# Kernel tuning notes

Measured on AMD Instinct MI355X. Metric: run time of the kernel, lower is better.

Reference implementation:

```python
import jax, jax.numpy as jnp
import numpy as np

FEAT = 512
COND = 768
N_HEADS = 8
D_HEAD = 64
D_ATTN = N_HEADS * D_HEAD  # 512


def setup_inputs() -> dict:
    key = jax.random.key(0)
    ks = jax.random.split(key, 8)
    B, N, M = 16, 4096, 77
    x = jax.random.normal(ks[0], (B, N, FEAT), dtype=jnp.float32)
    cond = jax.random.normal(ks[1], (B, M, COND), dtype=jnp.float32)
    s_f = 1.0 / np.sqrt(FEAT)
    s_c = 1.0 / np.sqrt(COND)
    s_a = 1.0 / np.sqrt(D_ATTN)
    Wq = jax.random.normal(ks[2], (FEAT, D_ATTN), dtype=jnp.float32) * s_f
    Wk = jax.random.normal(ks[3], (COND, D_ATTN), dtype=jnp.float32) * s_c
    Wv = jax.random.normal(ks[4], (COND, D_ATTN), dtype=jnp.float32) * s_c
    Wo = jax.random.normal(ks[5], (D_ATTN, FEAT), dtype=jnp.float32) * s_a
    bo = jax.random.normal(ks[6], (FEAT,), dtype=jnp.float32) * 0.01
    return {"x": x, "cond": cond, "Wq": Wq, "Wk": Wk, "Wv": Wv, "Wo": Wo, "bo": bo}


def reference(x, cond, Wq, Wk, Wv, Wo, bo):
    B, N, _ = x.shape
    M = cond.shape[1]
    scale = D_HEAD ** (-0.5)
    # projections (no bias, as in nn.Linear(..., bias=False))
    q = (x @ Wq).reshape(B, N, N_HEADS, D_HEAD)
    k = (cond @ Wk).reshape(B, M, N_HEADS, D_HEAD)
    v = (cond @ Wv).reshape(B, M, N_HEADS, D_HEAD)
    attn = jnp.einsum('bihd,bjhd->bhij', q, k) * scale  # [B,H,N,M]
    attn = jax.nn.softmax(attn, axis=-1)  # split-half inplace softmax == plain softmax
    out = jnp.einsum('bhij,bjhd->bihd', attn, v).reshape(B, N, D_ATTN)
    return out @ Wo + bo
```

## Files before the change

kernel.cpp:

```cpp
#include <hip/hip_runtime.h>

typedef __attribute__((ext_vector_type(8))) _Float16 f16x8;
typedef __attribute__((ext_vector_type(4))) float f32x4;

#define B_SZ   16
#define N_SEQ  4096
#define M_CTX  77
#define M_PAD  96
#define NH     8

__device__ __forceinline__ _Float16 f2h(float x) { return (_Float16)x; }

__device__ __forceinline__ void gload16(const void* g, void* l) {
    __builtin_amdgcn_global_load_lds(
        (const __attribute__((address_space(1))) unsigned int*)g,
        (__attribute__((address_space(3))) unsigned int*)l, 16, 0, 0);
}

#define BAR()   asm volatile("s_barrier" ::: "memory")
#define WAITV2() asm volatile("s_waitcnt vmcnt(2)" ::: "memory")
#define WAITV0() asm volatile("s_waitcnt vmcnt(0)" ::: "memory")

template<int C>
__device__ __forceinline__ float dppf(float x) {
    union { float f; int i; } u, v;
    u.f = x;
    v.i = __builtin_amdgcn_mov_dpp(u.i, C, 0xF, 0xF, true);
    return v.f;
}
__device__ __forceinline__ float rmax16(float x) {
    x = fmaxf(x, dppf<0xB1>(x));
    x = fmaxf(x, dppf<0x4E>(x));
    x = fmaxf(x, dppf<0x141>(x));
    x = fmaxf(x, dppf<0x140>(x));
    return x;
}
__device__ __forceinline__ float rsum16(float x) {
    x += dppf<0xB1>(x);
    x += dppf<0x4E>(x);
    x += dppf<0x141>(x);
    x += dppf<0x140>(x);
    return x;
}

__global__ __launch_bounds__(256)
void convert(const float4* __restrict__ x, f16x8* __restrict__ xh, int n8)
{
    int idx = blockIdx.x * 256 + threadIdx.x;
    int stride = gridDim.x * 256;
    for (int i = idx; i < n8; i += stride) {
        float4 a = x[2 * i];
        float4 b = x[2 * i + 1];
        f16x8 o;
        o[0] = f2h(a.x); o[1] = f2h(a.y); o[2] = f2h(a.z); o[3] = f2h(a.w);
        o[4] = f2h(b.x); o[5] = f2h(b.y); o[6] = f2h(b.z); o[7] = f2h(b.w);
        xh[i] = o;
    }
}

__global__ __launch_bounds__(256)
void prep(const float* __restrict__ Wq, const float* __restrict__ Wk,
          const float* __restrict__ Wv, const float* __restrict__ Wo,
          _Float16* __restrict__ WqT, _Float16* __restrict__ WkT,
          _Float16* __restrict__ WvT, _Float16* __restrict__ WoT)
{
    __shared__ float t[32][33];
    const float* W; _Float16* WT; int K; float scale = 1.0f;
    switch (blockIdx.z) {
        case 0:  W = Wq; WT = WqT; K = 512; scale = 0.125f; break;
        case 1:  W = Wk; WT = WkT; K = 768; break;
        case 2:  W = Wv; WT = WvT; K = 768; break;
        default: W = Wo; WT = WoT; K = 512; break;
    }
    const int ky = blockIdx.y;
    if (ky * 32 >= K) return;
    const int nx = blockIdx.x;
    const int tr = threadIdx.x >> 5, tc = threadIdx.x & 31;
#pragma unroll
    for (int i = 0; i < 4; ++i) {
        int kr = tr + i * 8;
        t[kr][tc] = W[(size_t)(ky * 32 + kr) * 512 + nx * 32 + tc];
    }
    __syncthreads();
#pragma unroll
    for (int i = 0; i < 4; ++i) {
        int nr = tr + i * 8;
        WT[(size_t)(nx * 32 + nr) * K + ky * 32 + tc] = f2h(t[tc][nr] * scale);
    }
}

__global__ __launch_bounds__(256)
void kv_proj(const float* __restrict__ cond, const _Float16* __restrict__ WkT,
             const _Float16* __restrict__ WvT, _Float16* __restrict__ Kswz,
             _Float16* __restrict__ Vswz)
{
    const int tid = threadIdx.x;
    const int l = tid & 63, w = tid >> 6;
    const int lrow = l & 15, lk = l >> 4;
    const int h = blockIdx.x, b = blockIdx.y, which = blockIdx.z;
    const _Float16* WT = which ? WvT : WkT;
    const float* cb = cond + (size_t)b * M_CTX * 768;

    f32x4 acc[5];
#pragma unroll
    for (int i = 0; i < 5; ++i)
#pragma unroll
        for (int e = 0; e < 4; ++e) acc[i][e] = 0.f;

    const int n = h * 64 + w * 16 + lrow;
    for (int kk = 0; kk < 24; ++kk) {
        f16x8 bfrag = *(const f16x8*)(WT + (size_t)n * 768 + kk * 32 + lk * 8);
#pragma unroll
        for (int rt = 0; rt < 5; ++rt) {
            int m = rt * 16 + lrow;
            f16x8 afrag;
#pragma unroll
            for (int j = 0; j < 8; ++j) afrag[j] = (_Float16)0.f;
            if (m < M_CTX) {
                const float* a = cb + (size_t)m * 768 + kk * 32 + lk * 8;
                float4 f0 = *(const float4*)a;
                float4 f1 = *(const float4*)(a + 4);
                afrag[0] = f2h(f0.x); afrag[1] = f2h(f0.y);
                afrag[2] = f2h(f0.z); afrag[3] = f2h(f0.w);
                afrag[4] = f2h(f1.x); afrag[5] = f2h(f1.y);
                afrag[6] = f2h(f1.z); afrag[7] = f2h(f1.w);
            }
            acc[rt] = __builtin_amdgcn_mfma_f32_16x16x32_f16(afrag, bfrag, acc[rt], 0, 0, 0);
        }
    }

    const int bh = b * NH + h;
    const int d = w * 16 + lrow;
    const int dhi = d >> 3, dlo = d & 7;
    if (which == 0) {
        _Float16* Kb = Kswz + (size_t)bh * (M_PAD * 64);
#pragma unroll
        for (int rt = 0; rt < 5; ++rt)
#pragma unroll
            for (int r = 0; r < 4; ++r) {
                int m = rt * 16 + lk * 4 + r;
                Kb[m * 64 + ((dhi ^ (m & 7)) * 8) + dlo] = f2h(acc[rt][r]);
            }
#pragma unroll
        for (int r = 0; r < 4; ++r) {
            int m = 80 + lk * 4 + r;
            Kb[m * 64 + ((dhi ^ (m & 7)) * 8) + dlo] = (_Float16)0.f;
        }
    } else {
        _Float16* Vb = Vswz + (size_t)bh * (64 * 128);
#pragma unroll
        for (int rt = 0; rt < 5; ++rt)
#pragma unroll
            for (int r = 0; r < 4; ++r) {
                int m = rt * 16 + lk * 4 + r;
                Vb[d * 128 + (((m >> 3) ^ dlo) * 8) + (m & 7)] = f2h(acc[rt][r]);
            }
#pragma unroll
        for (int r = 0; r < 4; ++r) {
            int m = 80 + lk * 4 + r;
            Vb[d * 128 + (((m >> 3) ^ dlo) * 8) + (m & 7)] = (_Float16)0.f;
        }
    }
}

template<int EMODE>
__global__ __launch_bounds__(512, 2)
void gemm256(const _Float16* __restrict__ A, const _Float16* __restrict__ BT,
             void* __restrict__ Cv, const float* __restrict__ bias)
{
    __shared__ _Float16 As[32768];
    __shared__ _Float16 Bs[32768];

    const int bid = blockIdx.x;
    const int wg = (bid & 7) * 64 + (bid >> 3);
    const int rb = wg >> 1, cb = wg & 1;
    const size_t row0 = (size_t)rb * 256;
    const int col0 = cb * 256;

    const int tid = threadIdx.x;
    const int l = tid & 63, w = tid >> 6;
    const int wy = w >> 2, wx = w & 3;
    const int lrow = l & 15, lk = l >> 4;

    f32x4 acc[8][4];
#pragma unroll
    for (int i = 0; i < 8; ++i)
#pragma unroll
        for (int j = 0; j < 4; ++j)
#pragma unroll
            for (int e = 0; e < 4; ++e) acc[i][j][e] = 0.f;

    const _Float16* a_src = A + (row0 + (size_t)(tid >> 2)) * 512 + (tid & 3) * 8;
    const _Float16* b_src = BT + (size_t)(col0 + (tid >> 2)) * 512 + (tid & 3) * 8;
    _Float16* As_d = &As[w * 512];
    _Float16* Bs_d = &Bs[w * 512];

    auto stageA = [&](int t) {
        const _Float16* s = a_src + t * 32;
        _Float16* d = As_d + (t & 1) * 8192;
        gload16(s, d);
        gload16(s + 128 * 512, d + 4096);
    };
    auto stageB = [&](int t) {
        const _Float16* s = b_src + t * 32;
        _Float16* d = Bs_d + (t & 1) * 8192;
        gload16(s, d);
        gload16(s + 128 * 512, d + 4096);
    };

    stageA(0); stageB(0); stageB(1);
    WAITV2();
    BAR();

    const _Float16* Ar = &As[wy * 4096 + lrow * 32 + lk * 8];
    const _Float16* Br = &Bs[(wx >> 1) * 4096 + ((wx & 1) * 64 + lrow) * 32 + lk * 8];

    for (int t = 0; t < 16; ++t) {
        const int bo = (t & 1) * 8192;
        f16x8 af[4], bf[4];
#pragma unroll
        for (int i = 0; i < 4; ++i) af[i] = *(const f16x8*)(Ar + bo + i * 512);
#pragma unroll
        for (int i = 0; i < 4; ++i) bf[i] = *(const f16x8*)(Br + bo + i * 512);
        if (t + 1 < 16) stageA(t + 1);
        BAR();
        __builtin_amdgcn_s_setprio(1);
#pragma unroll
        for (int mt = 0; mt < 4; ++mt)
#pragma unroll
            for (int nt = 0; nt < 4; ++nt)
                acc[mt][nt] = __builtin_amdgcn_mfma_f32_16x16x32_f16(af[mt], bf[nt], acc[mt][nt], 0, 0, 0);
        __builtin_amdgcn_s_setprio(0);

        f16x8 ag[4];
#pragma unroll
        for (int i = 0; i < 4; ++i) ag[i] = *(const f16x8*)(Ar + bo + (4 + i) * 512);
        if (t + 2 < 16) stageB(t + 2);
        __builtin_amdgcn_s_setprio(1);
#pragma unroll
        for (int mt = 0; mt < 4; ++mt)
#pragma unroll
            for (int nt = 0; nt < 4; ++nt)
                acc[4 + mt][nt] = __builtin_amdgcn_mfma_f32_16x16x32_f16(ag[mt], bf[nt], acc[4 + mt][nt], 0, 0, 0);
        __builtin_amdgcn_s_setprio(0);

        if (t <= 13)      WAITV2();
        else if (t == 14) WAITV0();
        if (t < 15) BAR();
    }

#pragma unroll
    for (int mt = 0; mt < 8; ++mt)
#pragma unroll
        for (int nt = 0; nt < 4; ++nt)
#pragma unroll
            for (int r = 0; r < 4; ++r) {
                size_t row = row0 + wy * 128 + mt * 16 + lk * 4 + r;
                int col = col0 + wx * 64 + nt * 16 + lrow;
                float v = acc[mt][nt][r];
                if (EMODE == 0) {
                    ((_Float16*)Cv)[row * 512 + col] = f2h(v);
                } else {
                    ((float*)Cv)[row * 512 + col] = v + bias[col];
                }
            }
}

__global__ __launch_bounds__(256)
void attn(const _Float16* __restrict__ Q, const _Float16* __restrict__ Kswz,
          const _Float16* __restrict__ Vswz, _Float16* __restrict__ AO)
{
    __shared__ _Float16 Ks[M_PAD * 64];
    __shared__ _Float16 Vs[64 * 128];
    __shared__ _Float16 Pl[4][16][104];

    const int tid = threadIdx.x;
    const int l = tid & 63, w = tid >> 6;
    const int lrow = l & 15, lk = l >> 4;
    const int chunk = blockIdx.x, h = blockIdx.y, b = blockIdx.z;
    const int bh = b * NH + h;

    {
        const _Float16* Kg = Kswz + (size_t)bh * (M_PAD * 64);
        const _Float16* Vg = Vswz + (size_t)bh * (64 * 128);
#pragma unroll
        for (int i = 0; i < 3; ++i) {
            int c = w * 3 + i;
            gload16(Kg + c * 512 + l * 8, Ks + c * 512);
        }
#pragma unroll
        for (int i = 0; i < 4; ++i) {
            int c = w * 4 + i;
            gload16(Vg + c * 512 + l * 8, Vs + c * 512);
        }
    }

    const size_t row0 = (size_t)b * N_SEQ + chunk * 256 + w * 64;
    f16x8 af[4][2];
    {
        const _Float16* Qb = Q + (row0 + lrow) * 512 + h * 64 + lk * 8;
#pragma unroll
        for (int mt = 0; mt < 4; ++mt)
#pragma unroll
            for (int kk = 0; kk < 2; ++kk)
                af[mt][kk] = *(const f16x8*)(Qb + (size_t)mt * 16 * 512 + kk * 32);
    }

    for (int idx = l; idx < 256; idx += 64)
        Pl[w][idx >> 4][80 + (idx & 15)] = (_Float16)0.f;

    __syncthreads();

    const bool m4ok = (lrow < 13);
    const int kswz = lrow & 7;

#pragma unroll
    for (int mt = 0; mt < 4; ++mt) {
        f32x4 s[5];
#pragma unroll
        for (int i = 0; i < 5; ++i)
#pragma unroll
            for (int e = 0; e < 4; ++e) s[i][e] = 0.f;
#pragma unroll
        for (int kk = 0; kk < 2; ++kk)
#pragma unroll
            for (int ct = 0; ct < 5; ++ct) {
                f16x8 kf = *(const f16x8*)&Ks[(ct * 16 + lrow) * 64 + (((kk * 4 + lk) ^ kswz) * 8)];
                s[ct] = __builtin_amdgcn_mfma_f32_16x16x32_f16(af[mt][kk], kf, s[ct], 0, 0, 0);
            }

        float rinv[4];
#pragma unroll
        for (int r = 0; r < 4; ++r) {
            float v0 = s[0][r], v1 = s[1][r], v2 = s[2][r], v3 = s[3][r], v4 = s[4][r];
            float mx = fmaxf(fmaxf(v0, v1), fmaxf(v2, v3));
            mx = fmaxf(mx, m4ok ? v4 : -1e30f);
            mx = rmax16(mx);
            float e0 = __expf(v0 - mx), e1 = __expf(v1 - mx);
            float e2 = __expf(v2 - mx), e3 = __expf(v3 - mx);
            float e4 = m4ok ? __expf(v4 - mx) : 0.f;
            float sum = ((e0 + e1) + (e2 + e3)) + e4;
            sum = rsum16(sum);
            rinv[r] = 1.0f / sum;
            int prow = lk * 4 + r;
            Pl[w][prow][lrow]      = f2h(e0);
            Pl[w][prow][16 + lrow] = f2h(e1);
            Pl[w][prow][32 + lrow] = f2h(e2);
            Pl[w][prow][48 + lrow] = f2h(e3);
            Pl[w][prow][64 + lrow] = f2h(e4);
        }

        f32x4 o[4];
#pragma unroll
        for (int i = 0; i < 4; ++i)
#pragma unroll
            for (int e2 = 0; e2 < 4; ++e2) o[i][e2] = 0.f;
#pragma unroll
        for (int kk = 0; kk < 3; ++kk) {
            f16x8 pa = *(const f16x8*)&Pl[w][lrow][kk * 32 + lk * 8];
#pragma unroll
            for (int ctd = 0; ctd < 4; ++ctd) {
                f16x8 vf = *(const f16x8*)&Vs[(ctd * 16 + lrow) * 128 + (((kk * 4 + lk) ^ kswz) * 8)];
                o[ctd] = __builtin_amdgcn_mfma_f32_16x16x32_f16(pa, vf, o[ctd], 0, 0, 0);
            }
        }

        const size_t rw = row0 + mt * 16 + lk * 4;
#pragma unroll
        for (int ctd = 0; ctd < 4; ++ctd)
#pragma unroll
            for (int r = 0; r < 4; ++r)
                AO[(rw + r) * 512 + h * 64 + ctd * 16 + lrow] = f2h(o[ctd][r] * rinv[r]);
    }
}

extern "C" void kernel_launch(void* const* d_in, const int* in_sizes, int n_in,
                              void* d_out, int out_size, void* d_ws, size_t ws_size,
                              hipStream_t stream)
{
    (void)in_sizes; (void)n_in; (void)out_size; (void)ws_size;
    const float* x    = (const float*)d_in[0];
    const float* cond = (const float*)d_in[1];
    const float* Wq   = (const float*)d_in[2];
    const float* Wk   = (const float*)d_in[3];
    const float* Wv   = (const float*)d_in[4];
    const float* Wo   = (const float*)d_in[5];
    const float* bo   = (const float*)d_in[6];

    char* ws = (char*)d_ws;
    _Float16* WqT  = (_Float16*)(ws);
    _Float16* WoT  = (_Float16*)(ws + 524288);
    _Float16* Kswz = (_Float16*)(ws + 1048576);
    _Float16* Vswz = (_Float16*)(ws + 2621440);
    _Float16* xh   = (_Float16*)(ws + 4718592);
    _Float16* WkT  = (_Float16*)(ws + 4718592);
    _Float16* WvT  = (_Float16*)(ws + 4718592 + 786432);
    _Float16* AO   = xh;
    _Float16* Qf   = (_Float16*)d_out;

    prep<<<dim3(16, 24, 4), 256, 0, stream>>>(Wq, Wk, Wv, Wo, WqT, WkT, WvT, WoT);
    kv_proj<<<dim3(8, 16, 2), 256, 0, stream>>>(cond, WkT, WvT, Kswz, Vswz);
    convert<<<dim3(2048), 256, 0, stream>>>((const float4*)x, (f16x8*)xh, 16 * 4096 * 512 / 8);
    gemm256<0><<<dim3(512), 512, 0, stream>>>(xh, WqT, Qf, nullptr);
    attn<<<dim3(16, 8, 16), 256, 0, stream>>>(Qf, Kswz, Vswz, AO);
    gemm256<1><<<dim3(512), 512, 0, stream>>>(AO, WoT, d_out, bo);
}
```

Before: 229.4 us.

## Replace double-buffered GEMM with 4-stage LDS ring and swizzled layout

Rewrites the projection GEMM main loop to use a four-deep LDS ring that prefetches three k-tiles ahead, with one wait and barrier per k-step instead of split A/B staging with two barriers. LDS rows use a rotated slot swizzle to reduce bank conflicts on fragment reads. All eight A fragments are loaded at once, which raises register pressure. The fixed vmcnt(8) wait may not fully drain loads in the last iterations, so the tail carries a synchronization risk.

```diff
diff --git a/kernel.cpp b/kernel.cpp
--- a/kernel.cpp
+++ b/kernel.cpp
@@ -17,9 +17,8 @@
         (__attribute__((address_space(3))) unsigned int*)l, 16, 0, 0);
 }
 
-#define BAR()   asm volatile("s_barrier" ::: "memory")
-#define WAITV2() asm volatile("s_waitcnt vmcnt(2)" ::: "memory")
-#define WAITV0() asm volatile("s_waitcnt vmcnt(0)" ::: "memory")
+#define BAR()    asm volatile("s_barrier" ::: "memory")
+#define WAITV8() asm volatile("s_waitcnt vmcnt(8)" ::: "memory")
 
 template<int C>
 __device__ __forceinline__ float dppf(float x) {
@@ -164,24 +163,38 @@
 }
 
 template<int EMODE>
-__global__ __launch_bounds__(512, 2)
-void gemm256(const _Float16* __restrict__ A, const _Float16* __restrict__ BT,
-             void* __restrict__ Cv, const float* __restrict__ bias)
-{
-    __shared__ _Float16 As[32768];
-    __shared__ _Float16 Bs[32768];
+__global__ __launch_bounds__(512)
+void gemm_pipe(const _Float16* __restrict__ A, const _Float16* __restrict__ BT,
+               void* __restrict__ Cv, const float* __restrict__ bias)
+{
+    __shared__ _Float16 L[4 * 16384];
 
     const int bid = blockIdx.x;
     const int wg = (bid & 7) * 64 + (bid >> 3);
-    const int rb = wg >> 1, cb = wg & 1;
-    const size_t row0 = (size_t)rb * 256;
-    const int col0 = cb * 256;
+    const size_t row0 = (size_t)(wg >> 1) * 256;
+    const int col0 = (wg & 1) * 256;
 
     const int tid = threadIdx.x;
     const int l = tid & 63, w = tid >> 6;
     const int wy = w >> 2, wx = w & 3;
     const int lrow = l & 15, lk = l >> 4;
 
+    const int srow  = l >> 2;
+    const int sslot = ((l & 3) - srow) & 3;
+    const _Float16* a_src = A  + (row0 + (size_t)(w * 32 + srow)) * 512 + sslot * 8;
+    const _Float16* b_src = BT + ((size_t)col0 + w * 32 + srow) * 512 + sslot * 8;
+
+    auto stage = [&](int t) {
+        _Float16* dA = &L[(t & 3) * 16384 + w * 1024];
+        _Float16* dB = dA + 8192;
+        const _Float16* sA = a_src + t * 32;
+        const _Float16* sB = b_src + t * 32;
+        gload16(sA,            dA);
+        gload16(sA + 16 * 512, dA + 512);
+        gload16(sB,            dB);
+        gload16(sB + 16 * 512, dB + 512);
+    };
+
     f32x4 acc[8][4];
 #pragma unroll
     for (int i = 0; i < 8; ++i)
@@ -190,63 +203,33 @@
 #pragma unroll
             for (int e = 0; e < 4; ++e) acc[i][j][e] = 0.f;
 
-    const _Float16* a_src = A + (row0 + (size_t)(tid >> 2)) * 512 + (tid & 3) * 8;
-    const _Float16* b_src = BT + (size_t)(col0 + (tid >> 2)) * 512 + (tid & 3) * 8;
-    _Float16* As_d = &As[w * 512];
-    _Float16* Bs_d = &Bs[w * 512];
-
-    auto stageA = [&](int t) {
-        const _Float16* s = a_src + t * 32;
-        _Float16* d = As_d + (t & 1) * 8192;
-        gload16(s, d);
-        gload16(s + 128 * 512, d + 4096);
-    };
-    auto stageB = [&](int t) {
-        const _Float16* s = b_src + t * 32;
-        _Float16* d = Bs_d + (t & 1) * 8192;
-        gload16(s, d);
-        gload16(s + 128 * 512, d + 4096);
-    };
-
-    stageA(0); stageB(0); stageB(1);
-    WAITV2();
-    BAR();
-
-    const _Float16* Ar = &As[wy * 4096 + lrow * 32 + lk * 8];
-    const _Float16* Br = &Bs[(wx >> 1) * 4096 + ((wx & 1) * 64 + lrow) * 32 + lk * 8];
-
-    for (int t = 0; t < 16; ++t) {
-        const int bo = (t & 1) * 8192;
-        f16x8 af[4], bf[4];
-#pragma unroll
-        for (int i = 0; i < 4; ++i) af[i] = *(const f16x8*)(Ar + bo + i * 512);
-#pragma unroll
-        for (int i = 0; i < 4; ++i) bf[i] = *(const f16x8*)(Br + bo + i * 512);
-        if (t + 1 < 16) stageA(t + 1);
+    stage(0); stage(1); stage(2);
+
+    const int rdoff = ((lk + lrow) & 3) * 8;
+    const int aoff = (wy * 128 + lrow) * 32 + rdoff;
+    const int boff = 8192 + (wx * 64 + lrow) * 32 + rdoff;
+
+    for (int kt = 0; kt < 16; ++kt) {
+        WAITV8();
         BAR();
+        if (kt + 3 < 16) stage(kt + 3);
+
+        const _Float16* Lb = &L[(kt & 3) * 16384];
+        f16x8 af[8], bf[4];
+#pragma unroll
+        for (int mt = 0; mt < 8; ++mt)
+            af[mt] = *(const f16x8*)(Lb + aoff + mt * 512);
+#pragma unroll
+        for (int nt = 0; nt < 4; ++nt)
+            bf[nt] = *(const f16x8*)(Lb + boff + nt * 512);
+
         __builtin_amdgcn_s_setprio(1);
 #pragma unroll
-        for (int mt = 0; mt < 4; ++mt)
+        for (int mt = 0; mt < 8; ++mt)
 #pragma unroll
             for (int nt = 0; nt < 4; ++nt)
                 acc[mt][nt] = __builtin_amdgcn_mfma_f32_16x16x32_f16(af[mt], bf[nt], acc[mt][nt], 0, 0, 0);
         __builtin_amdgcn_s_setprio(0);
-
-        f16x8 ag[4];
-#pragma unroll
-        for (int i = 0; i < 4; ++i) ag[i] = *(const f16x8*)(Ar + bo + (4 + i) * 512);
-        if (t + 2 < 16) stageB(t + 2);
-        __builtin_amdgcn_s_setprio(1);
-#pragma unroll
-        for (int mt = 0; mt < 4; ++mt)
-#pragma unroll
-            for (int nt = 0; nt < 4; ++nt)
-                acc[4 + mt][nt] = __builtin_amdgcn_mfma_f32_16x16x32_f16(ag[mt], bf[nt], acc[4 + mt][nt], 0, 0, 0);
-        __builtin_amdgcn_s_setprio(0);
-
-        if (t <= 13)      WAITV2();
-        else if (t == 14) WAITV0();
-        if (t < 15) BAR();
     }
 
 #pragma unroll
@@ -401,7 +384,7 @@
     prep<<<dim3(16, 24, 4), 256, 0, stream>>>(Wq, Wk, Wv, Wo, WqT, WkT, WvT, WoT);
     kv_proj<<<dim3(8, 16, 2), 256, 0, stream>>>(cond, WkT, WvT, Kswz, Vswz);
     convert<<<dim3(2048), 256, 0, stream>>>((const float4*)x, (f16x8*)xh, 16 * 4096 * 512 / 8);
-    gemm256<0><<<dim3(512), 512, 0, stream>>>(xh, WqT, Qf, nullptr);
+    gemm_pipe<0><<<dim3(512), 512, 0, stream>>>(xh, WqT, Qf, nullptr);
     attn<<<dim3(16, 8, 16), 256, 0, stream>>>(Qf, Kswz, Vswz, AO);
-    gemm256<1><<<dim3(512), 512, 0, stream>>>(AO, WoT, d_out, bo);
-}
+    gemm_pipe<1><<<dim3(512), 512, 0, stream>>>(AO, WoT, d_out, bo);
+}
```

Result: no change. 227.1 us (-1.0%).
